# Kernel optimization log

Hardware: AMD Instinct MI355X
Metric: run time of the kernel (lower is better)

## Reference

```python
import jax, jax.numpy as jnp
import numpy as np

N = 50000      # nodes
E = 625000     # edges
D_IN = 128     # in_feats
D_OUT = 128    # out_feats


def setup_inputs() -> dict:
    key = jax.random.key(0)
    k1, k2, k3, k4, k5, k6 = jax.random.split(key, 6)
    feat = jax.random.normal(k1, (N, D_IN), dtype=jnp.float32)
    affine = jax.random.uniform(k2, (E,), dtype=jnp.float32)
    src = jax.random.randint(k3, (E,), 0, N, dtype=jnp.int32)
    dst = jnp.sort(jax.random.randint(k4, (E,), 0, N, dtype=jnp.int32))
    # Linear(in_feats*2, out_feats): torch stores weight [out, in]; use [in, out] here
    bound = 1.0 / np.sqrt(2 * D_IN)
    W = jax.random.uniform(k5, (2 * D_IN, D_OUT), minval=-bound, maxval=bound, dtype=jnp.float32)
    b = jax.random.uniform(k6, (D_OUT,), minval=-bound, maxval=bound, dtype=jnp.float32)
    return {"feat": feat, "affine": affine, "src": src, "dst": dst, "W": W, "b": b}


def reference(feat, affine, src, dst, W, b):
    # u_mul_e: per-edge message = srcfeat[src] * edge scalar 'affine'
    msg = feat[src] * affine[:, None]                      # [E, D_IN]
    # fn.sum: scatter-add messages to destination nodes
    agg = jax.ops.segment_sum(msg, dst, num_segments=N)    # [N, D_IN]
    # concat dst features with aggregated neighborhood, then linear
    gcn_feat = jnp.concatenate([feat, agg], axis=-1)       # [N, 2*D_IN]
    return gcn_feat @ W + b                                # [N, D_OUT]
```

## Files before the change

### kernel.cpp

```cpp
#include <hip/hip_runtime.h>

#define N_NODES 50000
#define E_EDGES 625000
#define D 128

typedef __attribute__((ext_vector_type(8)))  short  short8;
typedef __attribute__((ext_vector_type(16))) float  floatx16;

static __device__ inline unsigned short f2bf(float f) {
    union { float f; unsigned u; } v; v.f = f;
    unsigned r = v.u + 0x7FFFu + ((v.u >> 16) & 1u);
    return (unsigned short)(r >> 16);
}
static __device__ inline float bflo(unsigned p) { return __uint_as_float(p << 16); }
static __device__ inline float bfhi(unsigned p) { return __uint_as_float(p & 0xFFFF0000u); }

__global__ __launch_bounds__(256) void prep_kernel(const int* __restrict__ dst,
                                                   const float* __restrict__ W,
                                                   const int* __restrict__ src,
                                                   const float* __restrict__ affine,
                                                   int* __restrict__ rowptr,
                                                   unsigned short* __restrict__ wimg,
                                                   uint2* __restrict__ meta) {
    int t = blockIdx.x * 256 + threadIdx.x;
    if (t < E_EDGES) {
        int d1 = dst[t];
        int d0 = (t == 0) ? -1 : dst[t - 1];
        for (int n = d0 + 1; n <= d1; ++n) rowptr[n] = t;
        if (t == E_EDGES - 1)
            for (int n = d1 + 1; n <= N_NODES; ++n) rowptr[n] = E_EDGES;
        uint2 m;
        m.x = (unsigned)src[t];
        m.y = __float_as_uint(affine[t]);
        meta[t] = m;
    }
    if (t < 4096) {
        int n = t & 127;
        int c = (t >> 7) & 15;
        int h = t >> 11;
        int krow = h * 128 + c * 8;
        short8 v;
        #pragma unroll
        for (int j = 0; j < 8; ++j)
            v[j] = (short)f2bf(W[(size_t)(krow + j) * D + n]);
        *((short8*)wimg + t) = v;
    }
}

#define NB_M 391

__global__ __launch_bounds__(256, 3) void gemm_mfma(const float* __restrict__ feat,
                                                    const unsigned short* __restrict__ wimg,
                                                    unsigned short* __restrict__ Z1b,
                                                    unsigned short* __restrict__ Y) {
    __shared__ short8 Bls[2048];

    int tid = threadIdx.x;
    int idx = blockIdx.x;
    int h   = (idx >> 3) & 1;
    int b   = ((idx >> 4) << 3) | (idx & 7);
    if (b >= NB_M) return;

    const short8* wsrc = (const short8*)wimg + h * 2048;
    #pragma unroll
    for (int i = 0; i < 8; ++i)
        Bls[tid + i * 256] = wsrc[tid + i * 256];

    int wave = tid >> 6;
    int lane = tid & 63;
    int m = lane & 31;
    int g = lane >> 5;
    int row0   = b * 128 + wave * 32;
    int row_a  = row0 + m;
    int rclamp = row_a < N_NODES ? row_a : 0;

    short8 fa[8];
    const float* ap = feat + (size_t)rclamp * D + g * 8;
    #pragma unroll
    for (int ks = 0; ks < 8; ++ks) {
        float4 u = *(const float4*)(ap + ks * 16);
        float4 v = *(const float4*)(ap + ks * 16 + 4);
        short8 a;
        a[0] = (short)f2bf(u.x); a[1] = (short)f2bf(u.y);
        a[2] = (short)f2bf(u.z); a[3] = (short)f2bf(u.w);
        a[4] = (short)f2bf(v.x); a[5] = (short)f2bf(v.y);
        a[6] = (short)f2bf(v.z); a[7] = (short)f2bf(v.w);
        fa[ks] = a;
    }
    __syncthreads();

    unsigned short* dstbuf = h ? Y : Z1b;

    #pragma unroll
    for (int t4 = 0; t4 < 4; ++t4) {
        int n = t4 * 32 + m;
        floatx16 acc = {0,0,0,0, 0,0,0,0, 0,0,0,0, 0,0,0,0};
        #pragma unroll
        for (int ks = 0; ks < 8; ++ks) {
            short8 bb = Bls[(ks * 2 + g) * 128 + n];
            acc = __builtin_amdgcn_mfma_f32_32x32x16_bf16(fa[ks], bb, acc, 0, 0, 0);
        }
        #pragma unroll
        for (int r = 0; r < 16; ++r) {
            int row = row0 + (r & 3) + 8 * (r >> 2) + 4 * g;
            if (row < N_NODES) dstbuf[(size_t)row * D + n] = f2bf(acc[r]);
        }
    }
}

__global__ __launch_bounds__(256) void agg_add(const unsigned short* __restrict__ Y,
                                               const unsigned short* __restrict__ Z1b,
                                               const uint2* __restrict__ meta,
                                               const int* __restrict__ rowptr,
                                               const float* __restrict__ bias,
                                               float* __restrict__ out) {
    int wave = threadIdx.x >> 6;
    int lane = threadIdx.x & 63;
    int n = blockIdx.x * 4 + wave;
    if (n >= N_NODES) return;
    int lo = rowptr[n], hi = rowptr[n + 1];
    int g  = lane >> 4;
    int jj = (lane & 15) << 3;
    const unsigned short* Yj = Y + jj;

    float acc[8] = {0,0,0,0,0,0,0,0};

    for (int e0 = lo; e0 < hi; e0 += 16) {
        uint2 md[4];
        #pragma unroll
        for (int u = 0; u < 4; ++u) {
            int i = e0 + u * 4 + g;
            md[u] = meta[i < hi ? i : lo];
        }
        float w[4];
        uint4 p[4];
        #pragma unroll
        for (int u = 0; u < 4; ++u) {
            int i = e0 + u * 4 + g;
            w[u] = (i < hi) ? __uint_as_float(md[u].y) : 0.f;
            p[u] = *(const uint4*)(Yj + (size_t)md[u].x * D);
        }
        #pragma unroll
        for (int u = 0; u < 4; ++u) {
            acc[0] += bflo(p[u].x) * w[u];  acc[1] += bfhi(p[u].x) * w[u];
            acc[2] += bflo(p[u].y) * w[u];  acc[3] += bfhi(p[u].y) * w[u];
            acc[4] += bflo(p[u].z) * w[u];  acc[5] += bfhi(p[u].z) * w[u];
            acc[6] += bflo(p[u].w) * w[u];  acc[7] += bfhi(p[u].w) * w[u];
        }
    }

    #pragma unroll
    for (int r = 0; r < 8; ++r) {
        acc[r] += __shfl_xor(acc[r], 16);
        acc[r] += __shfl_xor(acc[r], 32);
    }

    if (g == 0) {
        uint4  z  = *(const uint4*)(Z1b + (size_t)n * D + jj);
        float4 b0 = *(const float4*)(bias + jj);
        float4 b1 = *(const float4*)(bias + jj + 4);
        float* op = out + (size_t)n * D + jj;
        float4 o0, o1;
        o0.x = bflo(z.x) + b0.x + acc[0];  o0.y = bfhi(z.x) + b0.y + acc[1];
        o0.z = bflo(z.y) + b0.z + acc[2];  o0.w = bfhi(z.y) + b0.w + acc[3];
        o1.x = bflo(z.z) + b1.x + acc[4];  o1.y = bfhi(z.z) + b1.y + acc[5];
        o1.z = bflo(z.w) + b1.z + acc[6];  o1.w = bfhi(z.w) + b1.w + acc[7];
        *(float4*)op       = o0;
        *(float4*)(op + 4) = o1;
    }
}

extern "C" void kernel_launch(void* const* d_in, const int* in_sizes, int n_in,
                              void* d_out, int out_size, void* d_ws, size_t ws_size,
                              hipStream_t stream) {
    const float* feat   = (const float*)d_in[0];
    const float* affine = (const float*)d_in[1];
    const int*   src    = (const int*)  d_in[2];
    const int*   dst    = (const int*)  d_in[3];
    const float* W      = (const float*)d_in[4];
    const float* bias   = (const float*)d_in[5];
    float*       out    = (float*)d_out;

    unsigned short* wimg   = (unsigned short*)d_ws;
    int*            rowptr = (int*)((char*)d_ws + 65536);
    uint2*          meta   = (uint2*)((char*)d_ws + 266240);
    unsigned short* Y      = (unsigned short*)((char*)d_ws + 5267456);
    unsigned short* Z1b    = (unsigned short*)((char*)d_ws + 18067456);

    prep_kernel<<<(E_EDGES + 255) / 256, 256, 0, stream>>>(dst, W, src, affine,
                                                           rowptr, wimg, meta);
    int gemm_blocks = ((2 * NB_M + 15) / 16) * 16;
    gemm_mfma<<<gemm_blocks, 256, 0, stream>>>(feat, wimg, Z1b, Y);
    agg_add<<<(N_NODES + 3) / 4, 256, 0, stream>>>(Y, Z1b, meta, rowptr, bias, out);
}
```

Baseline: 127.8 us.

## Fuse edge preprocessing and weight conversion into GEMM kernel

Merges the prep kernel into the GEMM kernel. Each of the 391 blocks now builds the CSR rowptr and packs edge metadata for its slice of edges, converts the full fp32 weight matrix to bf16 directly into shared memory, and computes both output halves (Z1b and Y) itself. This removes one kernel launch and the global weight-image round trip, and reuses each block's A fragments across both halves. In exchange, every block redoes the full W conversion, LDS use doubles to 64KB, and grid parallelism drops from 784 to 391 blocks with launch bounds lowered to 2.

```diff
diff --git a/kernel.cpp b/kernel.cpp
--- a/kernel.cpp
+++ b/kernel.cpp
@@ -3,6 +3,8 @@
 #define N_NODES 50000
 #define E_EDGES 625000
 #define D 128
+#define NB_M 391
+#define EPB 1600
 
 typedef __attribute__((ext_vector_type(8)))  short  short8;
 typedef __attribute__((ext_vector_type(16))) float  floatx16;
@@ -15,56 +17,53 @@
 static __device__ inline float bflo(unsigned p) { return __uint_as_float(p << 16); }
 static __device__ inline float bfhi(unsigned p) { return __uint_as_float(p & 0xFFFF0000u); }
 
-__global__ __launch_bounds__(256) void prep_kernel(const int* __restrict__ dst,
-                                                   const float* __restrict__ W,
-                                                   const int* __restrict__ src,
-                                                   const float* __restrict__ affine,
-                                                   int* __restrict__ rowptr,
-                                                   unsigned short* __restrict__ wimg,
-                                                   uint2* __restrict__ meta) {
-    int t = blockIdx.x * 256 + threadIdx.x;
-    if (t < E_EDGES) {
-        int d1 = dst[t];
-        int d0 = (t == 0) ? -1 : dst[t - 1];
-        for (int n = d0 + 1; n <= d1; ++n) rowptr[n] = t;
-        if (t == E_EDGES - 1)
-            for (int n = d1 + 1; n <= N_NODES; ++n) rowptr[n] = E_EDGES;
-        uint2 m;
-        m.x = (unsigned)src[t];
-        m.y = __float_as_uint(affine[t]);
-        meta[t] = m;
+__global__ __launch_bounds__(256, 2) void gemm_fused(const float* __restrict__ feat,
+                                                     const float* __restrict__ W,
+                                                     const int* __restrict__ src,
+                                                     const int* __restrict__ dst,
+                                                     const float* __restrict__ affine,
+                                                     int* __restrict__ rowptr,
+                                                     uint2* __restrict__ meta,
+                                                     unsigned short* __restrict__ Z1b,
+                                                     unsigned short* __restrict__ Y) {
+    __shared__ short8 Bls[4096];
+
+    int tid = threadIdx.x;
+    int b   = blockIdx.x;
+
+    {
+        int e0 = b * EPB;
+        int e1 = e0 + EPB; if (e1 > E_EDGES) e1 = E_EDGES;
+        #pragma unroll
+        for (int i = 0; i < 7; ++i) {
+            int e = e0 + i * 256 + tid;
+            if (e < e1) {
+                int d1 = dst[e];
+                int d0 = (e == 0) ? -1 : dst[e - 1];
+                for (int n = d0 + 1; n <= d1; ++n) rowptr[n] = e;
+                if (e == E_EDGES - 1)
+                    for (int n = d1 + 1; n <= N_NODES; ++n) rowptr[n] = E_EDGES;
+                uint2 m;
+                m.x = (unsigned)src[e];
+                m.y = __float_as_uint(affine[e]);
+                meta[e] = m;
+            }
+        }
     }
-    if (t < 4096) {
-        int n = t & 127;
-        int c = (t >> 7) & 15;
-        int h = t >> 11;
+
+    #pragma unroll
+    for (int i = 0; i < 16; ++i) {
+        int s = tid + i * 256;
+        int n = s & 127;
+        int c = (s >> 7) & 15;
+        int h = s >> 11;
         int krow = h * 128 + c * 8;
         short8 v;
         #pragma unroll
         for (int j = 0; j < 8; ++j)
             v[j] = (short)f2bf(W[(size_t)(krow + j) * D + n]);
-        *((short8*)wimg + t) = v;
+        Bls[s] = v;
     }
-}
-
-#define NB_M 391
-
-__global__ __launch_bounds__(256, 3) void gemm_mfma(const float* __restrict__ feat,
-                                                    const unsigned short* __restrict__ wimg,
-                                                    unsigned short* __restrict__ Z1b,
-                                                    unsigned short* __restrict__ Y) {
-    __shared__ short8 Bls[2048];
-
-    int tid = threadIdx.x;
-    int idx = blockIdx.x;
-    int h   = (idx >> 3) & 1;
-    int b   = ((idx >> 4) << 3) | (idx & 7);
-    if (b >= NB_M) return;
-
-    const short8* wsrc = (const short8*)wimg + h * 2048;
-    #pragma unroll
-    for (int i = 0; i < 8; ++i)
-        Bls[tid + i * 256] = wsrc[tid + i * 256];
 
     int wave = tid >> 6;
     int lane = tid & 63;
@@ -89,17 +88,17 @@
     }
     __syncthreads();
 
-    unsigned short* dstbuf = h ? Y : Z1b;
-
     #pragma unroll
-    for (int t4 = 0; t4 < 4; ++t4) {
-        int n = t4 * 32 + m;
+    for (int t8 = 0; t8 < 8; ++t8) {
+        int h = t8 >> 2;
+        int n = (t8 & 3) * 32 + m;
         floatx16 acc = {0,0,0,0, 0,0,0,0, 0,0,0,0, 0,0,0,0};
         #pragma unroll
         for (int ks = 0; ks < 8; ++ks) {
-            short8 bb = Bls[(ks * 2 + g) * 128 + n];
+            short8 bb = Bls[h * 2048 + (ks * 2 + g) * 128 + n];
             acc = __builtin_amdgcn_mfma_f32_32x32x16_bf16(fa[ks], bb, acc, 0, 0, 0);
         }
+        unsigned short* dstbuf = h ? Y : Z1b;
         #pragma unroll
         for (int r = 0; r < 16; ++r) {
             int row = row0 + (r & 3) + 8 * (r >> 2) + 4 * g;
@@ -181,15 +180,12 @@
     const float* bias   = (const float*)d_in[5];
     float*       out    = (float*)d_out;
 
-    unsigned short* wimg   = (unsigned short*)d_ws;
-    int*            rowptr = (int*)((char*)d_ws + 65536);
-    uint2*          meta   = (uint2*)((char*)d_ws + 266240);
-    unsigned short* Y      = (unsigned short*)((char*)d_ws + 5267456);
-    unsigned short* Z1b    = (unsigned short*)((char*)d_ws + 18067456);
+    int*            rowptr = (int*)d_ws;
+    uint2*          meta   = (uint2*)((char*)d_ws + 262144);
+    unsigned short* Y      = (unsigned short*)((char*)d_ws + 5262144);
+    unsigned short* Z1b    = (unsigned short*)((char*)d_ws + 18062144);
 
-    prep_kernel<<<(E_EDGES + 255) / 256, 256, 0, stream>>>(dst, W, src, affine,
-                                                           rowptr, wimg, meta);
-    int gemm_blocks = ((2 * NB_M + 15) / 16) * 16;
-    gemm_mfma<<<gemm_blocks, 256, 0, stream>>>(feat, wimg, Z1b, Y);
+    gemm_fused<<<NB_M, 256, 0, stream>>>(feat, W, src, dst, affine,
+                                         rowptr, meta, Z1b, Y);
     agg_add<<<(N_NODES + 3) / 4, 256, 0, stream>>>(Y, Z1b, meta, rowptr, bias, out);
 }
```

New measurement: 131.9 us. 1.03x slower.
